# Kernel optimization log

Hardware: AMD Instinct MI355X
Metric: run time of the kernel (lower is better)

## Reference

```python
import jax, jax.numpy as jnp
import numpy as np

B, T, F = 64, 512, 256
ENC = 256      # encoder output dim
P = 128        # projection_dim
H = 256        # gru_hidden_dim
K = 12         # num_future_steps
TEMP = 0.1


def setup_inputs() -> dict:
    key = jax.random.key(0)
    ks = jax.random.split(key, 12)
    s = lambda *d: 1.0 / np.sqrt(d[0])
    return {
        "x_seq": jax.random.normal(ks[0], (B, T, F), jnp.float32),
        # encoder: Dense(F -> ENC)
        "W_enc": jax.random.normal(ks[1], (F, ENC), jnp.float32) * s(F),
        "b_enc": jnp.zeros((ENC,), jnp.float32),
        # projection: Dense(ENC -> P)
        "W_proj": jax.random.normal(ks[2], (ENC, P), jnp.float32) * s(ENC),
        "b_proj": jnp.zeros((P,), jnp.float32),
        # GRUCell (flax convention: input dense has bias, hidden dense bias only on n)
        "Wi": jax.random.normal(ks[3], (P, 3 * H), jnp.float32) * s(P),
        "bi": jnp.zeros((3 * H,), jnp.float32),
        "Wh": jax.random.normal(ks[4], (H, 3 * H), jnp.float32) * s(H),
        "bhn": jnp.zeros((H,), jnp.float32),
        # K predictors: Dense(H -> P)
        "Wp": jax.random.normal(ks[5], (K, H, P), jnp.float32) * s(H),
        "bp": jnp.zeros((K, P), jnp.float32),
    }


def _gru_scan(z_seq, Wi, bi, Wh, bhn):
    # z_seq: [B, T, P] -> c_seq: [B, T, H]
    def step(h, x_t):
        gi = x_t @ Wi + bi          # [B, 3H]
        gh = h @ Wh                 # [B, 3H]
        ir, iz, inn = jnp.split(gi, 3, axis=-1)
        hr, hz, hn = jnp.split(gh, 3, axis=-1)
        r = jax.nn.sigmoid(ir + hr)
        z = jax.nn.sigmoid(iz + hz)
        n = jnp.tanh(inn + r * (hn + bhn))
        h_new = (1.0 - z) * n + z * h
        return h_new, h_new

    h0 = jnp.zeros((z_seq.shape[0], Wh.shape[0]), z_seq.dtype)
    _, c = jax.lax.scan(step, h0, jnp.swapaxes(z_seq, 0, 1))  # c: [T, B, H]
    return jnp.swapaxes(c, 0, 1)


def reference(x_seq, W_enc, b_enc, W_proj, b_proj, Wi, bi, Wh, bhn, Wp, bp):
    # encoder per timestep (vmap(vmap(Dense)) == batched matmul)
    z_seq = x_seq @ W_enc + b_enc                 # [B, T, ENC]
    z_seq = z_seq @ W_proj + b_proj               # [B, T, P]
    c_seq = _gru_scan(z_seq, Wi, bi, Wh, bhn)     # [B, T, H]

    Tlen = z_seq.shape[1]
    loss = jnp.asarray(0.0, z_seq.dtype)
    for k in range(1, K + 1):
        if Tlen - k <= 0:
            continue
        z_pos = z_seq[:, k:]                      # [B, T-k, P]
        pred = c_seq[:, :-k] @ Wp[k - 1] + bp[k - 1]  # [B, T-k, P]
        logits = jnp.einsum('btd,bkd->btk', pred, z_pos) / TEMP
        labels = jnp.arange(logits.shape[1])
        # NOTE: faithful to source: [..., labels] with labels=arange is an
        # identity gather along the last axis (not a diagonal pick).
        loss = loss + jnp.mean(-jax.nn.log_softmax(logits, axis=-1)[..., labels])
    return loss / K
```

## Files before the change

kernel.cpp:

```cpp
#include <hip/hip_runtime.h>
#include <hip/hip_bf16.h>
#include <math.h>

#define B_   64
#define T_   512
#define F_   256
#define ENC_ 256
#define P_   128
#define H_   256
#define K_   12
#define INV_TEMP 10.0f
#define NT_  3072

typedef unsigned short u16;
typedef _Float16 half2v __attribute__((ext_vector_type(2)));
union U2H { unsigned int u; half2v h; };
typedef __attribute__((ext_vector_type(8))) short bf16x8;
typedef __attribute__((ext_vector_type(4))) float f32x4;
typedef _Float16 f16x8 __attribute__((ext_vector_type(8)));
union BF8 { bf16x8 v; u16 e[8]; };

__device__ __forceinline__ float rcpf(float x) {
#if __has_builtin(__builtin_amdgcn_rcpf)
    return __builtin_amdgcn_rcpf(x);
#else
    return 1.f / x;
#endif
}
__device__ __forceinline__ u16 f2bf(float f) {
    unsigned int u = __float_as_uint(f);
    unsigned int r = (u + 0x7fffu + ((u >> 16) & 1u)) >> 16;
    return (u16)r;
}
__device__ __forceinline__ float bf2f(u16 v) {
    return __uint_as_float(((unsigned int)v) << 16);
}
__device__ __forceinline__ float bflo(unsigned int u) { return __uint_as_float(u << 16); }
__device__ __forceinline__ float bfhi(unsigned int u) { return __uint_as_float(u & 0xffff0000u); }
__device__ __forceinline__ float wave_sum(float v) {
    #pragma unroll
    for (int o = 32; o > 0; o >>= 1) v += __shfl_down(v, o, 64);
    return v;
}

__global__ __launch_bounds__(256) void setup_conv(const float* __restrict__ Wh,
                                                  _Float16* __restrict__ Wht,
                                                  const float* __restrict__ Wi,
                                                  u16* __restrict__ Wit,
                                                  const float* __restrict__ Wp,
                                                  u16* __restrict__ Wpt,
                                                  const float* __restrict__ We,
                                                  const float* __restrict__ be,
                                                  const float* __restrict__ Wpj,
                                                  const float* __restrict__ bpj,
                                                  u16* __restrict__ Wct,
                                                  float* __restrict__ bc,
                                                  float* __restrict__ accum) {
    int bid = blockIdx.x;
    if (bid < 192) {
        __shared__ float tile0[32][33];
        int g0 = (bid % 24) * 32, k0 = (bid / 24) * 32;
        int tx = threadIdx.x & 31, ty = threadIdx.x >> 5;
        #pragma unroll
        for (int i = 0; i < 32; i += 8)
            tile0[ty + i][tx] = Wh[(size_t)(k0 + ty + i) * 768 + g0 + tx];
        __syncthreads();
        #pragma unroll
        for (int i = 0; i < 32; i += 8)
            Wht[(size_t)(g0 + ty + i) * 256 + k0 + tx] = (_Float16)tile0[tx][ty + i];
    } else if (bid < 288) {
        __shared__ float tile[32][33];
        int b2 = bid - 192;
        int n0 = (b2 % 24) * 32, k0 = (b2 / 24) * 32;
        int tx = threadIdx.x & 31, ty = threadIdx.x >> 5;
        #pragma unroll
        for (int i = 0; i < 32; i += 8)
            tile[ty + i][tx] = Wi[(size_t)(k0 + ty + i) * 768 + n0 + tx];
        __syncthreads();
        #pragma unroll
        for (int i = 0; i < 32; i += 8)
            Wit[(size_t)(n0 + ty + i) * 128 + k0 + tx] = f2bf(tile[tx][ty + i]);
    } else if (bid < 672) {
        __shared__ float tile2[32][33];
        int b3 = bid - 288;
        int kq = b3 / 32, rem = b3 % 32;
        int h0 = (rem % 8) * 32, p0 = (rem / 8) * 32;
        int tx = threadIdx.x & 31, ty = threadIdx.x >> 5;
        #pragma unroll
        for (int i = 0; i < 32; i += 8)
            tile2[ty + i][tx] = Wp[(size_t)kq * H_ * P_ + (size_t)(h0 + ty + i) * P_ + p0 + tx];
        __syncthreads();
        #pragma unroll
        for (int i = 0; i < 32; i += 8)
            Wpt[(size_t)kq * P_ * H_ + (size_t)(p0 + ty + i) * H_ + h0 + tx] = f2bf(tile2[tx][ty + i]);
    } else {
        int f = (bid - 672) * 2 + (threadIdx.x >> 7);
        int p = threadIdx.x & 127;
        if (f < F_) {
            float a = 0.f;
            for (int e = 0; e < ENC_; e++) a = fmaf(We[f * ENC_ + e], Wpj[e * P_ + p], a);
            Wct[(size_t)p * F_ + f] = f2bf(a);
        } else if (f == F_) {
            float a = bpj[p];
            for (int e = 0; e < ENC_; e++) a = fmaf(be[e], Wpj[e * P_ + p], a);
            bc[p] = a;
        } else {
            #pragma unroll
            for (int i = 0; i < 8; i++) accum[p * 8 + i] = 0.f;
        }
    }
}

__global__ __launch_bounds__(256) void gemm_mfma_f32a(const float* __restrict__ A,
                                                      const u16* __restrict__ Bt,
                                                      const float* __restrict__ bias,
                                                      u16* __restrict__ Ch,
                                                      int N, int K) {
    int tid  = threadIdx.x;
    int w    = tid >> 6;
    int lane = tid & 63;
    int col  = lane & 15;
    int quad = lane >> 4;
    int bm = blockIdx.y * 64, bn = blockIdx.x * 128;

    f32x4 acc[8] = {};
    const float* arow = A + (size_t)(bm + w * 16 + col) * K;
    #pragma unroll
    for (int k0 = 0; k0 < K; k0 += 32) {
        float4 v0 = *(const float4*)(arow + k0 + quad * 8);
        float4 v1 = *(const float4*)(arow + k0 + quad * 8 + 4);
        BF8 af;
        af.e[0] = f2bf(v0.x); af.e[1] = f2bf(v0.y); af.e[2] = f2bf(v0.z); af.e[3] = f2bf(v0.w);
        af.e[4] = f2bf(v1.x); af.e[5] = f2bf(v1.y); af.e[6] = f2bf(v1.z); af.e[7] = f2bf(v1.w);
        #pragma unroll
        for (int nt = 0; nt < 8; nt++) {
            bf16x8 bf = *(const bf16x8*)(Bt + (size_t)(bn + nt * 16 + col) * K + k0 + quad * 8);
            acc[nt] = __builtin_amdgcn_mfma_f32_16x16x32_bf16(af.v, bf, acc[nt], 0, 0, 0);
        }
    }
    #pragma unroll
    for (int nt = 0; nt < 8; nt++) {
        int gn = bn + nt * 16 + col;
        float bv = bias[gn];
        #pragma unroll
        for (int r = 0; r < 4; r++) {
            int gm = bm + w * 16 + quad * 4 + r;
            Ch[(size_t)gm * N + gn] = f2bf(acc[nt][r] + bv);
        }
    }
}

__global__ __launch_bounds__(256) void gemm_mfma(const u16* __restrict__ A,
                                                 const u16* __restrict__ Bt,
                                                 const float* __restrict__ bias,
                                                 u16* __restrict__ Ch,
                                                 int N, int K) {
    int tid  = threadIdx.x;
    int w    = tid >> 6;
    int lane = tid & 63;
    int col  = lane & 15;
    int quad = lane >> 4;
    int bm = blockIdx.y * 64, bn = blockIdx.x * 128;

    f32x4 acc[8] = {};
    const u16* arow = A + (size_t)(bm + w * 16 + col) * K;
    #pragma unroll
    for (int k0 = 0; k0 < K; k0 += 32) {
        bf16x8 af = *(const bf16x8*)(arow + k0 + quad * 8);
        #pragma unroll
        for (int nt = 0; nt < 8; nt++) {
            bf16x8 bf = *(const bf16x8*)(Bt + (size_t)(bn + nt * 16 + col) * K + k0 + quad * 8);
            acc[nt] = __builtin_amdgcn_mfma_f32_16x16x32_bf16(af, bf, acc[nt], 0, 0, 0);
        }
    }
    #pragma unroll
    for (int nt = 0; nt < 8; nt++) {
        int gn = bn + nt * 16 + col;
        float bv = bias[gn];
        #pragma unroll
        for (int r = 0; r < 4; r++) {
            int gm = bm + w * 16 + quad * 4 + r;
            Ch[(size_t)gm * N + gn] = f2bf(acc[nt][r] + bv);
        }
    }
}

__global__ __attribute__((amdgpu_flat_work_group_size(512, 512)))
void gru_zsum_loss(const u16* __restrict__ gi,
                   const _Float16* __restrict__ Wht,
                   const float* __restrict__ bhn,
                   u16* __restrict__ ch,
                   const u16* __restrict__ zh,
                   float* __restrict__ zsum,
                   const u16* __restrict__ Wpt,
                   const float* __restrict__ bp,
                   float* __restrict__ accum) {
    __shared__ __align__(16) char smem[52804];
    int tid  = threadIdx.x;
    int bid  = blockIdx.x;
    int lane = tid & 63, w = tid >> 6;
    int col  = lane & 15, quad = lane >> 4;
    int* progress = (int*)(accum + 512);
    int* zflagA   = progress + 64;
    int* qctr     = progress + 128;

    if (bid < 64) {
        _Float16* hbase = (_Float16*)smem;
        int b   = bid;
        int jj0 = w * 32 + col;

        f16x8 wf[3][2][8];
        #pragma unroll
        for (int g = 0; g < 3; g++)
            #pragma unroll
            for (int n2 = 0; n2 < 2; n2++) {
                const _Float16* src = Wht + (size_t)(g * 256 + jj0 + n2 * 16) * 256 + quad * 8;
                #pragma unroll
                for (int k0 = 0; k0 < 8; k0++)
                    wf[g][n2][k0] = *(const f16x8*)(src + k0 * 32);
            }
        #pragma unroll
        for (int g = 0; g < 3; g++)
            #pragma unroll
            for (int n2 = 0; n2 < 2; n2++)
                #pragma unroll
                for (int k0 = 0; k0 < 8; k0++)
                    asm volatile("" : "+v"(wf[g][n2][k0]));

        for (int i = tid; i < 528; i += 512) hbase[i] = (_Float16)0.f;

        const u16* gb = gi + (size_t)b * T_ * 768;
        u16* cb       = ch + (size_t)b * T_ * 256;
        float bh0 = bhn[jj0], bh1 = bhn[jj0 + 16];
        float hold0 = 0.f, hold1 = 0.f;
        unsigned int pf[6];
        pf[0] = gb[jj0];        pf[1] = gb[jj0 + 16];
        pf[2] = gb[256 + jj0];  pf[3] = gb[256 + jj0 + 16];
        pf[4] = gb[512 + jj0];  pf[5] = gb[512 + jj0 + 16];
        __syncthreads();

        auto body = [&](int t, int c) {
            int n = c ^ 1;
            const _Float16* HC = hbase + c * 264;
            _Float16*       HN = hbase + n * 264;
            f32x4 aR0 = {}, aR1 = {}, aZ0 = {}, aZ1 = {}, aN0 = {}, aN1 = {};
            #pragma unroll
            for (int k0 = 0; k0 < 8; k0++) {
                f16x8 af = *(const f16x8*)(HC + k0 * 32 + quad * 8);
                aR0 = __builtin_amdgcn_mfma_f32_16x16x32_f16(af, wf[0][0][k0], aR0, 0, 0, 0);
                aR1 = __builtin_amdgcn_mfma_f32_16x16x32_f16(af, wf[0][1][k0], aR1, 0, 0, 0);
                aZ0 = __builtin_amdgcn_mfma_f32_16x16x32_f16(af, wf[1][0][k0], aZ0, 0, 0, 0);
                aZ1 = __builtin_amdgcn_mfma_f32_16x16x32_f16(af, wf[1][1][k0], aZ1, 0, 0, 0);
                aN0 = __builtin_amdgcn_mfma_f32_16x16x32_f16(af, wf[2][0][k0], aN0, 0, 0, 0);
                aN1 = __builtin_amdgcn_mfma_f32_16x16x32_f16(af, wf[2][1][k0], aN1, 0, 0, 0);
            }
            float rg0 = rcpf(1.f + __expf(-(bf2f((u16)pf[0]) + aR0[0])));
            float rg1 = rcpf(1.f + __expf(-(bf2f((u16)pf[1]) + aR1[0])));
            float zg0 = rcpf(1.f + __expf(-(bf2f((u16)pf[2]) + aZ0[0])));
            float zg1 = rcpf(1.f + __expf(-(bf2f((u16)pf[3]) + aZ1[0])));
            float xn0 = bf2f((u16)pf[4]) + rg0 * (aN0[0] + bh0);
            float xn1 = bf2f((u16)pf[5]) + rg1 * (aN1[0] + bh1);
            float nn0 = fmaf(2.f, rcpf(1.f + __expf(-2.f * xn0)), -1.f);
            float nn1 = fmaf(2.f, rcpf(1.f + __expf(-2.f * xn1)), -1.f);
            hold0 = (1.f - zg0) * nn0 + zg0 * hold0;
            hold1 = (1.f - zg1) * nn1 + zg1 * hold1;
            if (quad == 0) {
                HN[jj0]      = (_Float16)hold0;
                HN[jj0 + 16] = (_Float16)hold1;
            } else if (quad == 1) {
                u16* cr = cb + (size_t)t * 256;
                cr[jj0]      = f2bf(hold0);
                cr[jj0 + 16] = f2bf(hold1);
            }
            if (t + 1 < T_) {
                const u16* gr = gb + (size_t)(t + 1) * 768;
                pf[0] = gr[jj0];        pf[1] = gr[jj0 + 16];
                pf[2] = gr[256 + jj0];  pf[3] = gr[256 + jj0 + 16];
                pf[4] = gr[512 + jj0];  pf[5] = gr[512 + jj0 + 16];
            }
            asm volatile("s_waitcnt lgkmcnt(0)" ::: "memory");
            __builtin_amdgcn_s_barrier();
            asm volatile("" ::: "memory");
        };

        #pragma unroll 1
        for (int t = 0; t < T_; t += 2) {
            body(t,     0);
            body(t + 1, 1);
            if (((t + 2) & 127) == 0) {
                asm volatile("s_waitcnt vmcnt(0)" ::: "memory");
                __syncthreads();
                if (tid == 0) {
                    __threadfence();
                    __hip_atomic_store(progress + b, t + 2,
                                       __ATOMIC_RELEASE, __HIP_MEMORY_SCOPE_AGENT);
                }
            }
        }
    } else if (bid < 128) {
        float (*part)[128] = (float (*)[128])smem;
        int b  = bid - 64;
        int pg = tid & 31;
        int g  = tid >> 5;
        const u16* zb = zh + (size_t)b * T_ * P_;
        float s0 = 0.f, s1 = 0.f, s2 = 0.f, s3 = 0.f;
        for (int t = 1 + g; t < T_; t += 16) {
            uint2 v = *(const uint2*)(zb + (size_t)t * P_ + pg * 4);
            s0 += bflo(v.x); s1 += bfhi(v.x);
            s2 += bflo(v.y); s3 += bfhi(v.y);
        }
        part[g][pg * 4 + 0] = s0; part[g][pg * 4 + 1] = s1;
        part[g][pg * 4 + 2] = s2; part[g][pg * 4 + 3] = s3;
        __syncthreads();
        if (tid < 128) {
            float s = 0.f;
            #pragma unroll
            for (int g2 = 0; g2 < 16; g2++) s += part[g2][tid];
            zsum[(size_t)b * P_ + tid] = s;
        }
        asm volatile("s_waitcnt vmcnt(0)" ::: "memory");
        __syncthreads();
        if (tid == 0) {
            __threadfence();
            __hip_atomic_store(zflagA + b, 1, __ATOMIC_RELEASE, __HIP_MEMORY_SCOPE_AGENT);
        }
    }

    u16 (*Pst)[136] = (u16 (*)[136])smem;
    u16 (*Zt)[136]  = (u16 (*)[136])(smem + 34816);
    float* sS       = (float*)(smem + 52224);
    float* red      = (float*)(smem + 52736);
    int*   sTile    = (int*)(smem + 52768);

    while (true) {
        if (tid == 0) *sTile = atomicAdd(qctr, 1);
        __syncthreads();
        int tile = *sTile;
        __syncthreads();
        if (tile >= NT_) break;

        int t0i = tile / 768;
        int rem = tile - t0i * 768;
        int b   = rem & 63;
        int kz  = rem >> 6;
        int k   = kz + 1;
        int t0  = t0i * 128;
        int Tk  = T_ - k;
        int need = (t0i + 1) << 7;
        if (tid == 0) {
            while (__hip_atomic_load(zflagA + b, __ATOMIC_ACQUIRE, __HIP_MEMORY_SCOPE_AGENT) == 0)
                __builtin_amdgcn_s_sleep(2);
            while (__hip_atomic_load(progress + b, __ATOMIC_ACQUIRE, __HIP_MEMORY_SCOPE_AGENT) < need)
                __builtin_amdgcn_s_sleep(2);
        }
        __syncthreads();

        const u16* zb = zh + (size_t)b * T_ * P_;

        if (tid < 128) {
            float s = zsum[(size_t)b * P_ + tid];
            for (int t = 1; t < k; t++) s -= bf2f(zb[(size_t)t * P_ + tid]);
            sS[tid] = s;
        }

        {
            f32x4 acc[8] = {};
            const u16* arow = ch + ((size_t)b * T_ + t0 + w * 16 + col) * H_;
            const u16* wk   = Wpt + (size_t)(k - 1) * P_ * H_;
            #pragma unroll
            for (int k0 = 0; k0 < 8; k0++) {
                bf16x8 af = *(const bf16x8*)(arow + k0 * 32 + quad * 8);
                #pragma unroll
                for (int nt = 0; nt < 8; nt++) {
                    bf16x8 bf = *(const bf16x8*)(wk + (size_t)(nt * 16 + col) * H_ + k0 * 32 + quad * 8);
                    acc[nt] = __builtin_amdgcn_mfma_f32_16x16x32_bf16(af, bf, acc[nt], 0, 0, 0);
                }
            }
            #pragma unroll
            for (int nt = 0; nt < 8; nt++) {
                float bias = bp[(size_t)(k - 1) * P_ + nt * 16 + col];
                #pragma unroll
                for (int r = 0; r < 4; r++)
                    Pst[w * 16 + quad * 4 + r][nt * 16 + col] = f2bf(acc[nt][r] + bias);
            }
        }
        __syncthreads();

        float mloc[4], sloc[4];
        #pragma unroll
        for (int r = 0; r < 4; r++) { mloc[r] = -INFINITY; sloc[r] = 0.f; }

        for (int ct = 0; ct < Tk; ct += 64) {
            __syncthreads();
            {
                int cc = tid;
                #pragma unroll
                for (int rep = 0; rep < 2; rep++, cc += 512) {
                    int row = cc >> 4;
                    int off = (cc & 15) * 8;
                    int tcol = k + ct + row;
                    *(uint4*)&Zt[row][off] = *(const uint4*)(zb + (size_t)tcol * P_ + off);
                }
            }
            __syncthreads();
            f32x4 acc[4] = {};
            #pragma unroll
            for (int k0 = 0; k0 < 4; k0++) {
                bf16x8 af = *(const bf16x8*)(&Pst[w * 16 + col][k0 * 32 + quad * 8]);
                #pragma unroll
                for (int nt = 0; nt < 4; nt++) {
                    bf16x8 bf = *(const bf16x8*)(&Zt[nt * 16 + col][k0 * 32 + quad * 8]);
                    acc[nt] = __builtin_amdgcn_mfma_f32_16x16x32_bf16(af, bf, acc[nt], 0, 0, 0);
                }
            }
            #pragma unroll
            for (int r = 0; r < 4; r++) {
                float l[4];
                float tmax = -INFINITY;
                #pragma unroll
                for (int nt = 0; nt < 4; nt++) {
                    bool valid = (ct + nt * 16 + col) < Tk;
                    l[nt] = valid ? acc[nt][r] * INV_TEMP : -INFINITY;
                    tmax = fmaxf(tmax, l[nt]);
                }
                float mnew = fmaxf(mloc[r], tmax);
                float e = __expf(l[0] - mnew) + __expf(l[1] - mnew)
                        + __expf(l[2] - mnew) + __expf(l[3] - mnew);
                sloc[r] = sloc[r] * __expf(mloc[r] - mnew) + e;
                mloc[r] = mnew;
            }
        }
        #pragma unroll
        for (int r = 0; r < 4; r++) {
            #pragma unroll
            for (int o = 1; o < 16; o <<= 1) {
                float mo = __shfl_xor(mloc[r], o, 64);
                float so = __shfl_xor(sloc[r], o, 64);
                float mn = fmaxf(mloc[r], mo);
                sloc[r] = sloc[r] * __expf(mloc[r] - mn) + so * __expf(mo - mn);
                mloc[r] = mn;
            }
        }
        float tkinv = INV_TEMP / (float)Tk;
        float scale = 1.0f / ((float)K_ * (float)B_ * (float)Tk);
        float bs = 0.f;
        #pragma unroll
        for (int r = 0; r < 4; r++) {
            int row = w * 16 + quad * 4 + r;
            BF8 pv;
            pv.v = *(const bf16x8*)(&Pst[row][col * 8]);
            float d = 0.f;
            #pragma unroll
            for (int m = 0; m < 8; m++) d = fmaf(bf2f(pv.e[m]), sS[col * 8 + m], d);
            #pragma unroll
            for (int o = 1; o < 16; o <<= 1) d += __shfl_xor(d, o, 64);
            int gr = t0 + row;
            if (gr < Tk) bs += mloc[r] + __logf(sloc[r]) - d * tkinv;
        }
        if (col != 0) bs = 0.f;
        bs = wave_sum(bs);
        if (lane == 0) red[w] = bs;
        __syncthreads();
        if (tid == 0) {
            float tot = 0.f;
            #pragma unroll
            for (int i = 0; i < 8; i++) tot += red[i];
            atomicAdd(&accum[(t0i * 809 + b * 67 + kz * 131) & 511], tot * scale);
        }
        __syncthreads();
    }
}

__global__ void finalize(const float* __restrict__ accum, float* __restrict__ out) {
    int tid = threadIdx.x;
    __shared__ float red[4];
    float v = 0.f;
    for (int i = tid; i < 512; i += 256) v += accum[i];
    float sres = wave_sum(v);
    if ((tid & 63) == 0) red[tid >> 6] = sres;
    __syncthreads();
    if (tid == 0) out[0] = red[0] + red[1] + red[2] + red[3];
}

extern "C" void kernel_launch(void* const* d_in, const int* in_sizes, int n_in,
                              void* d_out, int out_size, void* d_ws, size_t ws_size,
                              hipStream_t stream) {
    const float* x      = (const float*)d_in[0];
    const float* W_enc  = (const float*)d_in[1];
    const float* b_enc  = (const float*)d_in[2];
    const float* W_proj = (const float*)d_in[3];
    const float* b_proj = (const float*)d_in[4];
    const float* Wi     = (const float*)d_in[5];
    const float* bi     = (const float*)d_in[6];
    const float* Wh     = (const float*)d_in[7];
    const float* bhn    = (const float*)d_in[8];
    const float* Wp     = (const float*)d_in[9];
    const float* bp     = (const float*)d_in[10];
    float* out = (float*)d_out;

    float* ws    = (float*)d_ws;
    float* bc    = ws;
    float* accum = bc + 128;
    _Float16* Wht = (_Float16*)(ws + 1152);
    u16* Wct     = (u16*)(ws + 99456);
    u16* Wit     = (u16*)(ws + 115840);
    u16* Wpt     = (u16*)(ws + 164992);
    u16* zh      = (u16*)(ws + 361600);
    float* zsum  = ws + 2458752;
    u16* gi      = (u16*)(ws + 2466944);
    u16* ch      = (u16*)(ws + 15049856);

    const int MT = B_ * T_;

    setup_conv<<<801, 256, 0, stream>>>(Wh, Wht, Wi, Wit, Wp, Wpt,
                                        W_enc, b_enc, W_proj, b_proj, Wct, bc, accum);
    gemm_mfma_f32a<<<dim3(1, MT / 64), 256, 0, stream>>>(x, Wct, bc, zh, P_, F_);
    gemm_mfma<<<dim3(6, MT / 64), 256, 0, stream>>>(zh, Wit, bi, gi, 3 * H_, P_);
    gru_zsum_loss<<<256, 512, 0, stream>>>(gi, Wht, bhn, ch, zh, zsum, Wpt, bp, accum);
    finalize<<<1, 256, 0, stream>>>(accum, out);
}
```

Baseline: 990.1 us.

## Pack four batch rows per GRU block and prefetch Z tiles into registers

The GRU recurrence now runs four batch rows per workgroup, one per MFMA quad row-group, using 16 blocks instead of 64. Each block now does useful work in all 16 MFMA rows and frees CUs for the loss tiles. The loss tile ordering now maps tiles to (b, k) with k varying fastest. The Z-tile global loads are software-prefetched into registers one iteration ahead. The risk is that each GRU step still has the same serial latency while the per-block h stores and LDS traffic grow, and the tile reorder changes how well loss work overlaps with GRU progress.

```diff
diff --git a/kernel.cpp b/kernel.cpp
--- a/kernel.cpp
+++ b/kernel.cpp
@@ -11,6 +11,7 @@
 #define K_   12
 #define INV_TEMP 10.0f
 #define NT_  3072
+#define GRUB_ 16
 
 typedef unsigned short u16;
 typedef _Float16 half2v __attribute__((ext_vector_type(2)));
@@ -204,9 +205,9 @@
     int* zflagA   = progress + 64;
     int* qctr     = progress + 128;
 
-    if (bid < 64) {
+    if (bid < GRUB_) {
         _Float16* hbase = (_Float16*)smem;
-        int b   = bid;
+        int bb  = bid * 4;
         int jj0 = w * 32 + col;
 
         f16x8 wf[3][2][8];
@@ -227,10 +228,10 @@
                 for (int k0 = 0; k0 < 8; k0++)
                     asm volatile("" : "+v"(wf[g][n2][k0]));
 
-        for (int i = tid; i < 528; i += 512) hbase[i] = (_Float16)0.f;
-
-        const u16* gb = gi + (size_t)b * T_ * 768;
-        u16* cb       = ch + (size_t)b * T_ * 256;
+        for (int i = tid; i < 2176; i += 512) hbase[i] = (_Float16)0.f;
+
+        const u16* gb = gi + (size_t)(bb + quad) * T_ * 768;
+        u16* cb       = ch + (size_t)(bb + quad) * T_ * 256;
         float bh0 = bhn[jj0], bh1 = bhn[jj0 + 16];
         float hold0 = 0.f, hold1 = 0.f;
         unsigned int pf[6];
@@ -241,12 +242,13 @@
 
         auto body = [&](int t, int c) {
             int n = c ^ 1;
-            const _Float16* HC = hbase + c * 264;
-            _Float16*       HN = hbase + n * 264;
+            const _Float16* HC = hbase + c * 1088;
+            _Float16*       HN = hbase + n * 1088;
             f32x4 aR0 = {}, aR1 = {}, aZ0 = {}, aZ1 = {}, aN0 = {}, aN1 = {};
+            const _Float16* ha = HC + (col >> 2) * 272 + quad * 8;
             #pragma unroll
             for (int k0 = 0; k0 < 8; k0++) {
-                f16x8 af = *(const f16x8*)(HC + k0 * 32 + quad * 8);
+                f16x8 af = *(const f16x8*)(ha + k0 * 32);
                 aR0 = __builtin_amdgcn_mfma_f32_16x16x32_f16(af, wf[0][0][k0], aR0, 0, 0, 0);
                 aR1 = __builtin_amdgcn_mfma_f32_16x16x32_f16(af, wf[0][1][k0], aR1, 0, 0, 0);
                 aZ0 = __builtin_amdgcn_mfma_f32_16x16x32_f16(af, wf[1][0][k0], aZ0, 0, 0, 0);
@@ -264,14 +266,11 @@
             float nn1 = fmaf(2.f, rcpf(1.f + __expf(-2.f * xn1)), -1.f);
             hold0 = (1.f - zg0) * nn0 + zg0 * hold0;
             hold1 = (1.f - zg1) * nn1 + zg1 * hold1;
-            if (quad == 0) {
-                HN[jj0]      = (_Float16)hold0;
-                HN[jj0 + 16] = (_Float16)hold1;
-            } else if (quad == 1) {
-                u16* cr = cb + (size_t)t * 256;
-                cr[jj0]      = f2bf(hold0);
-                cr[jj0 + 16] = f2bf(hold1);
-            }
+            HN[quad * 272 + jj0]      = (_Float16)hold0;
+            HN[quad * 272 + jj0 + 16] = (_Float16)hold1;
+            u16* cr = cb + (size_t)t * 256;
+            cr[jj0]      = f2bf(hold0);
+            cr[jj0 + 16] = f2bf(hold1);
             if (t + 1 < T_) {
                 const u16* gr = gb + (size_t)(t + 1) * 768;
                 pf[0] = gr[jj0];        pf[1] = gr[jj0 + 16];
@@ -292,14 +291,16 @@
                 __syncthreads();
                 if (tid == 0) {
                     __threadfence();
-                    __hip_atomic_store(progress + b, t + 2,
-                                       __ATOMIC_RELEASE, __HIP_MEMORY_SCOPE_AGENT);
+                    #pragma unroll
+                    for (int i = 0; i < 4; i++)
+                        __hip_atomic_store(progress + bb + i, t + 2,
+                                           __ATOMIC_RELEASE, __HIP_MEMORY_SCOPE_AGENT);
                 }
             }
         }
-    } else if (bid < 128) {
+    } else if (bid < GRUB_ + 64) {
         float (*part)[128] = (float (*)[128])smem;
-        int b  = bid - 64;
+        int b  = bid - GRUB_;
         int pg = tid & 31;
         int g  = tid >> 5;
         const u16* zb = zh + (size_t)b * T_ * P_;
@@ -341,8 +342,8 @@
 
         int t0i = tile / 768;
         int rem = tile - t0i * 768;
-        int b   = rem & 63;
-        int kz  = rem >> 6;
+        int b   = rem / 12;
+        int kz  = rem - b * 12;
         int k   = kz + 1;
         int t0  = t0i * 128;
         int Tk  = T_ - k;
@@ -390,19 +391,22 @@
         #pragma unroll
         for (int r = 0; r < 4; r++) { mloc[r] = -INFINITY; sloc[r] = 0.f; }
 
+        int row0 = tid >> 4;
+        int row1 = row0 + 32;
+        int off  = (tid & 15) * 8;
+        uint4 rA = *(const uint4*)(zb + (size_t)(k + row0) * P_ + off);
+        uint4 rB = *(const uint4*)(zb + (size_t)(k + row1) * P_ + off);
+
         for (int ct = 0; ct < Tk; ct += 64) {
             __syncthreads();
-            {
-                int cc = tid;
-                #pragma unroll
-                for (int rep = 0; rep < 2; rep++, cc += 512) {
-                    int row = cc >> 4;
-                    int off = (cc & 15) * 8;
-                    int tcol = k + ct + row;
-                    *(uint4*)&Zt[row][off] = *(const uint4*)(zb + (size_t)tcol * P_ + off);
-                }
-            }
+            *(uint4*)&Zt[row0][off] = rA;
+            *(uint4*)&Zt[row1][off] = rB;
             __syncthreads();
+            if (ct + 64 < Tk) {
+                int tc = k + ct + 64;
+                rA = *(const uint4*)(zb + (size_t)(tc + row0) * P_ + off);
+                rB = *(const uint4*)(zb + (size_t)(tc + row1) * P_ + off);
+            }
             f32x4 acc[4] = {};
             #pragma unroll
             for (int k0 = 0; k0 < 4; k0++) {
```

Measured after the change: 1.136 ms. 14.7% more time.
